# Performance work log

Hardware: AMD Instinct MI355X
Metric: run time of the kernel (lower is better)

## Reference

```python
import jax, jax.numpy as jnp
import numpy as np

N_HEADS = 16

def setup_inputs() -> dict:
    key = jax.random.key(0)
    ks = jax.random.split(key, 5)
    D = 1024
    B, T = 4, 1024
    scale = 1.0 / np.sqrt(D)
    x = jax.random.normal(ks[0], (B, T, D), dtype=jnp.float32)
    Wq = jax.random.normal(ks[1], (D, D), dtype=jnp.float32) * scale
    Wk = jax.random.normal(ks[2], (D, D), dtype=jnp.float32) * scale
    Wv = jax.random.normal(ks[3], (D, D), dtype=jnp.float32) * scale
    Wo = jax.random.normal(ks[4], (D, D), dtype=jnp.float32) * scale
    return {"x": x, "Wq": Wq, "Wk": Wk, "Wv": Wv, "Wo": Wo}


def reference(x, Wq, Wk, Wv, Wo):
    # FLA BasedLinearAttention (mode='chunk', normalize=True, scale=1) with
    # Taylor feature map phi(u) = [1, u/d^{1/4}, (u (x) u)/sqrt(2 d)], so
    # phi(q)·phi(k) = 1 + s + s^2/2 where s = (q·k)/sqrt(d).
    B, T, D = x.shape
    H = N_HEADS
    d = D // H  # head_dim == feature_dim
    # torch Linear: y = x @ W.T (bias=False in FLA proj layers)
    q = (x @ Wq.T).reshape(B, T, H, d).transpose(0, 2, 1, 3)  # b h t d
    k = (x @ Wk.T).reshape(B, T, H, d).transpose(0, 2, 1, 3)
    v = (x @ Wv.T).reshape(B, T, H, d).transpose(0, 2, 1, 3)
    s = jnp.einsum('bhtd,bhsd->bhts', q, k) / jnp.sqrt(jnp.float32(d))
    scores = 1.0 + s + 0.5 * s * s  # always > 0 (= ((s+1)^2+1)/2)
    causal = jnp.tril(jnp.ones((T, T), dtype=bool))
    scores = jnp.where(causal, scores, 0.0)
    num = jnp.einsum('bhts,bhsd->bhtd', scores, v)
    den = jnp.sum(scores, axis=-1, keepdims=True)
    o = num / den  # b h t d
    o = o.transpose(0, 2, 1, 3).reshape(B, T, D)  # b t (h d)
    return o @ Wo.T
```

## Files before the change

kernel.cpp:

```cpp
#include <hip/hip_runtime.h>

typedef unsigned short u16;
typedef __attribute__((ext_vector_type(8))) short bf16x8;
typedef __attribute__((ext_vector_type(8))) unsigned short u16x8;
typedef __attribute__((ext_vector_type(4))) float f32x4;

#define MFMA16(a, b, c) __builtin_amdgcn_mfma_f32_16x16x32_bf16((a), (b), (c), 0, 0, 0)

__device__ __forceinline__ void gll16(const void* g, void* l) {
    __builtin_amdgcn_global_load_lds(
        (const __attribute__((address_space(1))) unsigned int*)g,
        (__attribute__((address_space(3))) unsigned int*)l, 16, 0, 0);
}

__device__ __forceinline__ u16 f2b(float f) {
    unsigned int u = __float_as_uint(f);
    u += 0x7fffu + ((u >> 16) & 1u);
    return (u16)(u >> 16);
}

__device__ __forceinline__ unsigned int pkbf(float a, float b) {
    return (unsigned int)f2b(a) | ((unsigned int)f2b(b) << 16);
}

__global__ __launch_bounds__(256) void cast_x(const float* __restrict__ s,
                                              u16* __restrict__ d) {
    int i = (blockIdx.x * 256 + threadIdx.x) * 8;
    float4 a = *(const float4*)(s + i);
    float4 b = *(const float4*)(s + i + 4);
    uint4 r = make_uint4(pkbf(a.x, a.y), pkbf(a.z, a.w),
                         pkbf(b.x, b.y), pkbf(b.z, b.w));
    *(uint4*)(d + i) = r;
}

__global__ __launch_bounds__(256) void cast_w(const float* __restrict__ w0,
                                              const float* __restrict__ w1,
                                              const float* __restrict__ w2,
                                              const float* __restrict__ w3,
                                              u16* __restrict__ base) {
    const float* s = (blockIdx.y == 0) ? w0 : (blockIdx.y == 1) ? w1
                    : (blockIdx.y == 2) ? w2 : w3;
    u16* d = base + (size_t)blockIdx.y * 1048576;
    int i = (blockIdx.x * 256 + threadIdx.x) * 8;
    float4 a = *(const float4*)(s + i);
    float4 b = *(const float4*)(s + i + 4);
    uint4 r = make_uint4(pkbf(a.x, a.y), pkbf(a.z, a.w),
                         pkbf(b.x, b.y), pkbf(b.z, b.w));
    *(uint4*)(d + i) = r;
}

template <int BN, int OUT_BF16>
__global__ __launch_bounds__(256) void gemm_bt(const u16* __restrict__ A,
                                               const u16* __restrict__ W,
                                               void* __restrict__ Yv,
                                               int M, int N, int K) {
    __shared__ u16 As[128 * 32];
    __shared__ u16 Bs[BN * 32];
    constexpr int MI = (BN == 128) ? 4 : 2;
    const int t = threadIdx.x, w = t >> 6, lane = t & 63;
    const int quad = lane >> 4, m16 = lane & 15;
    const int wr = (BN == 128) ? ((w >> 1) * 64) : (w * 32);
    const int wc = (BN == 128) ? ((w & 1) * 64) : 0;
    const int row0 = blockIdx.x * 128, col0 = blockIdx.y * BN;
    const int srow = lane >> 2;
    const int scol = (lane & 3) * 8;

    f32x4 acc[MI][4];
#pragma unroll
    for (int i = 0; i < MI; ++i)
#pragma unroll
        for (int j = 0; j < 4; ++j) acc[i][j] = (f32x4){0.f, 0.f, 0.f, 0.f};

    for (int k0 = 0; k0 < K; k0 += 32) {
        if constexpr (BN == 128) {
#pragma unroll
            for (int cc = 0; cc < 2; ++cc) {
                const int c = w * 2 + cc;
                const int rr = c * 16 + srow;
                gll16(A + (size_t)(row0 + rr) * K + k0 + scol, &As[c * 512]);
                gll16(W + (size_t)(col0 + rr) * K + k0 + scol, &Bs[c * 512]);
            }
        } else {
#pragma unroll
            for (int cc = 0; cc < 2; ++cc) {
                const int c = w * 2 + cc;
                const int rr = c * 16 + srow;
                gll16(A + (size_t)(row0 + rr) * K + k0 + scol, &As[c * 512]);
            }
            {
                const int rr = w * 16 + srow;
                gll16(W + (size_t)(col0 + rr) * K + k0 + scol, &Bs[w * 512]);
            }
        }
        __syncthreads();
        bf16x8 af[MI], bf[4];
#pragma unroll
        for (int i = 0; i < MI; ++i)
            af[i] = *(const bf16x8*)&As[(wr + i * 16 + m16) * 32 + quad * 8];
#pragma unroll
        for (int j = 0; j < 4; ++j)
            bf[j] = *(const bf16x8*)&Bs[(wc + j * 16 + m16) * 32 + quad * 8];
#pragma unroll
        for (int i = 0; i < MI; ++i)
#pragma unroll
            for (int j = 0; j < 4; ++j) acc[i][j] = MFMA16(af[i], bf[j], acc[i][j]);
        __syncthreads();
    }
#pragma unroll
    for (int i = 0; i < MI; ++i)
#pragma unroll
        for (int j = 0; j < 4; ++j)
#pragma unroll
            for (int r = 0; r < 4; ++r) {
                const int rg = row0 + wr + i * 16 + quad * 4 + r;
                const int cg = col0 + wc + j * 16 + m16;
                if (OUT_BF16)
                    ((u16*)Yv)[(size_t)rg * N + cg] = f2b(acc[i][j][r]);
                else
                    ((float*)Yv)[(size_t)rg * N + cg] = acc[i][j][r];
            }
}

__global__ __launch_bounds__(256) void transpose_v(const u16* __restrict__ v,
                                                   u16* __restrict__ vT, int vstride) {
    __shared__ u16 tile[64][72];
    const int t = threadIdx.x;
    const int tt = blockIdx.x, h = blockIdx.y, b = blockIdx.z;
    {
        const int row = t >> 2, c4 = (t & 3) * 16;
        const u16* src = v + (size_t)(b * 1024 + tt * 64 + row) * vstride + h * 64 + c4;
        *(u16x8*)&tile[row][c4] = *(const u16x8*)src;
        *(u16x8*)&tile[row][c4 + 8] = *(const u16x8*)(src + 8);
    }
    __syncthreads();
    const int vd = t >> 2, tk = (t & 3) * 16;
    u16 tmp[16];
#pragma unroll
    for (int j = 0; j < 16; ++j) tmp[j] = tile[tk + j][vd];
    u16* dst = vT + (size_t)((b * 16 + h) * 64 + vd) * 1024 + tt * 64 + tk;
    *(u16x8*)dst = *(u16x8*)tmp;
    *(u16x8*)(dst + 8) = *(u16x8*)(tmp + 8);
}

__global__ __launch_bounds__(256) void based_attn(const u16* __restrict__ q,
                                                  const u16* __restrict__ k,
                                                  const u16* __restrict__ vT,
                                                  u16* __restrict__ o) {
    __shared__ u16 qs[2][128][32];
    __shared__ u16 ks[2][64][32];
    __shared__ u16 vs[2][64][32];
    __shared__ u16 Ss[2][128][32];

    const int t = threadIdx.x, w = t >> 6, lane = t & 63;
    const int quad = lane >> 4, m16 = lane & 15;
    const int qt2 = 7 - blockIdx.x;
    const int h = blockIdx.y, b = blockIdx.z;
    const int Q0 = qt2 * 128;
    const int srow = lane >> 2, s8 = (lane & 3) * 8;
    const int qw0 = Q0 + w * 32;

#pragma unroll
    for (int cc = 0; cc < 4; ++cc) {
        const int c = w * 4 + cc;
        const int dblk = c >> 3, rr = (c & 7) * 16 + srow;
        gll16(q + (size_t)(b * 1024 + Q0 + rr) * 3072 + h * 64 + dblk * 32 + s8,
              &qs[dblk][(c & 7) * 16][0]);
    }

    bf16x8 ones;
#pragma unroll
    for (int e = 0; e < 8; ++e) ones[e] = (short)0x3F80;

    f32x4 num[2][4], den[2];
#pragma unroll
    for (int i = 0; i < 2; ++i) {
        den[i] = (f32x4){0.f, 0.f, 0.f, 0.f};
#pragma unroll
        for (int j = 0; j < 4; ++j) num[i][j] = (f32x4){0.f, 0.f, 0.f, 0.f};
    }

    const int ktmax = 2 * qt2 + 1;
    for (int kt = 0; kt <= ktmax; ++kt) {
#pragma unroll
        for (int cc = 0; cc < 2; ++cc) {
            const int c = w * 2 + cc;
            const int blk = c >> 2, rr = (c & 3) * 16 + srow;
            gll16(k + (size_t)(b * 1024 + kt * 64 + rr) * 3072 + h * 64 + blk * 32 + s8,
                  &ks[blk][(c & 3) * 16][0]);
            gll16(vT + (size_t)((b * 16 + h) * 64 + rr) * 1024 + kt * 64 + blk * 32 + s8,
                  &vs[blk][(c & 3) * 16][0]);
        }
        __syncthreads();

        const bool active = (kt * 64 <= qw0 + 31);
        if (active) {
            f32x4 sacc[2][4];
#pragma unroll
            for (int iq = 0; iq < 2; ++iq)
#pragma unroll
                for (int jk = 0; jk < 4; ++jk) sacc[iq][jk] = (f32x4){0.f, 0.f, 0.f, 0.f};
#pragma unroll
            for (int kd = 0; kd < 2; ++kd) {
                bf16x8 af[4], qf[2];
#pragma unroll
                for (int jk = 0; jk < 4; ++jk)
                    af[jk] = *(const bf16x8*)&ks[kd][jk * 16 + m16][quad * 8];
#pragma unroll
                for (int iq = 0; iq < 2; ++iq)
                    qf[iq] = *(const bf16x8*)&qs[kd][w * 32 + iq * 16 + m16][quad * 8];
#pragma unroll
                for (int iq = 0; iq < 2; ++iq)
#pragma unroll
                    for (int jk = 0; jk < 4; ++jk)
                        sacc[iq][jk] = MFMA16(af[jk], qf[iq], sacc[iq][jk]);
            }
            const bool needMask = (kt * 64 + 63 > qw0);
#pragma unroll
            for (int iq = 0; iq < 2; ++iq) {
                const int qglob = qw0 + iq * 16 + m16;
#pragma unroll
                for (int jk = 0; jk < 4; ++jk) {
                    const int key0 = kt * 64 + jk * 16 + quad * 4;
                    float sc[4];
#pragma unroll
                    for (int r = 0; r < 4; ++r) {
                        const float u = fmaf(sacc[iq][jk][r], 0.125f, 1.0f);
                        sc[r] = fmaf(u * 0.5f, u, 0.5f);
                    }
                    if (needMask) {
#pragma unroll
                        for (int r = 0; r < 4; ++r)
                            if (key0 + r > qglob) sc[r] = 0.f;
                    }
                    const int kl = jk * 16 + quad * 4;
                    *(uint2*)&Ss[kl >> 5][w * 32 + iq * 16 + m16][kl & 31] =
                        make_uint2(pkbf(sc[0], sc[1]), pkbf(sc[2], sc[3]));
                }
            }
#pragma unroll
            for (int kb = 0; kb < 2; ++kb) {
                bf16x8 sf[2], vf[4];
#pragma unroll
                for (int i = 0; i < 2; ++i)
                    sf[i] = *(const bf16x8*)&Ss[kb][w * 32 + i * 16 + m16][quad * 8];
#pragma unroll
                for (int j = 0; j < 4; ++j)
                    vf[j] = *(const bf16x8*)&vs[kb][j * 16 + m16][quad * 8];
#pragma unroll
                for (int i = 0; i < 2; ++i) {
#pragma unroll
                    for (int j = 0; j < 4; ++j) num[i][j] = MFMA16(sf[i], vf[j], num[i][j]);
                    den[i] = MFMA16(sf[i], ones, den[i]);
                }
            }
        }
        __syncthreads();
    }

#pragma unroll
    for (int i = 0; i < 2; ++i)
#pragma unroll
        for (int r = 0; r < 4; ++r) {
            const float inv = 1.0f / den[i][r];
            const int tok = b * 1024 + Q0 + w * 32 + i * 16 + quad * 4 + r;
#pragma unroll
            for (int j = 0; j < 4; ++j)
                o[(size_t)tok * 1024 + h * 64 + j * 16 + m16] = f2b(num[i][j][r] * inv);
        }
}

extern "C" void kernel_launch(void* const* d_in, const int* in_sizes, int n_in,
                              void* d_out, int out_size, void* d_ws, size_t ws_size,
                              hipStream_t stream) {
    const float* x  = (const float*)d_in[0];
    const float* Wq = (const float*)d_in[1];
    const float* Wk = (const float*)d_in[2];
    const float* Wv = (const float*)d_in[3];
    const float* Wo = (const float*)d_in[4];
    float* out = (float*)d_out;

    const size_t MEL = 4096ull * 1024ull;
    u16* xb   = (u16*)d_ws;
    u16* Wqkv = xb + MEL;
    u16* Wob  = Wqkv + 3ull * 1024 * 1024;
    u16* qkv  = Wob + 1024ull * 1024;
    u16* vT   = qkv + 3ull * MEL;
    u16* o    = vT + MEL;

    cast_x<<<2048, 256, 0, stream>>>(x, xb);
    cast_w<<<dim3(512, 4), 256, 0, stream>>>(Wq, Wk, Wv, Wo, Wqkv);

    dim3 gq(32, 24);
    gemm_bt<128, 1><<<gq, 256, 0, stream>>>(xb, Wqkv, qkv, 4096, 3072, 1024);

    dim3 gt(16, 16, 4);
    transpose_v<<<gt, 256, 0, stream>>>(qkv + 2048, vT, 3072);

    dim3 ga(8, 16, 4);
    based_attn<<<ga, 256, 0, stream>>>(qkv, qkv + 1024, vT, o);

    dim3 go(32, 16);
    gemm_bt<64, 0><<<go, 256, 0, stream>>>(o, Wob, (void*)out, 4096, 1024, 1024);
}
```

Baseline: 187.3 us.

## Fuse casts, write V transposed from QKV GEMM, pair causal tiles in attention

Merges the x and weight cast kernels into one launch. The QKV GEMM epilogue now writes Q/K into a compact buffer and stores V directly in transposed layout, which removes the separate transpose kernel. The attention kernel now has each block own two 64-row query tiles (p and 15-p) so causal work is balanced across blocks, and it double-buffers K/V loads into LDS to overlap them with compute. The changes cut launches and global traffic, at the cost of strided uncoalesced 8-byte V stores and smaller per-wave query tiles.

```diff
diff --git a/kernel.cpp b/kernel.cpp
--- a/kernel.cpp
+++ b/kernel.cpp
@@ -23,37 +23,35 @@
     return (unsigned int)f2b(a) | ((unsigned int)f2b(b) << 16);
 }
 
-__global__ __launch_bounds__(256) void cast_x(const float* __restrict__ s,
-                                              u16* __restrict__ d) {
-    int i = (blockIdx.x * 256 + threadIdx.x) * 8;
+__global__ __launch_bounds__(256) void cast_all(const float* __restrict__ x,
+                                                const float* __restrict__ w0,
+                                                const float* __restrict__ w1,
+                                                const float* __restrict__ w2,
+                                                const float* __restrict__ w3,
+                                                u16* __restrict__ xb,
+                                                u16* __restrict__ wb) {
+    const int bid = blockIdx.x;
+    const float* s; u16* d; int off;
+    if (bid < 2048) { s = x; d = xb; off = bid; }
+    else {
+        const int wi = (bid - 2048) >> 9;
+        s = (wi == 0) ? w0 : (wi == 1) ? w1 : (wi == 2) ? w2 : w3;
+        d = wb + (size_t)wi * 1048576;
+        off = (bid - 2048) & 511;
+    }
+    const int i = (off * 256 + threadIdx.x) * 8;
     float4 a = *(const float4*)(s + i);
     float4 b = *(const float4*)(s + i + 4);
-    uint4 r = make_uint4(pkbf(a.x, a.y), pkbf(a.z, a.w),
-                         pkbf(b.x, b.y), pkbf(b.z, b.w));
-    *(uint4*)(d + i) = r;
-}
-
-__global__ __launch_bounds__(256) void cast_w(const float* __restrict__ w0,
-                                              const float* __restrict__ w1,
-                                              const float* __restrict__ w2,
-                                              const float* __restrict__ w3,
-                                              u16* __restrict__ base) {
-    const float* s = (blockIdx.y == 0) ? w0 : (blockIdx.y == 1) ? w1
-                    : (blockIdx.y == 2) ? w2 : w3;
-    u16* d = base + (size_t)blockIdx.y * 1048576;
-    int i = (blockIdx.x * 256 + threadIdx.x) * 8;
-    float4 a = *(const float4*)(s + i);
-    float4 b = *(const float4*)(s + i + 4);
-    uint4 r = make_uint4(pkbf(a.x, a.y), pkbf(a.z, a.w),
-                         pkbf(b.x, b.y), pkbf(b.z, b.w));
-    *(uint4*)(d + i) = r;
-}
-
-template <int BN, int OUT_BF16>
+    *(uint4*)(d + i) = make_uint4(pkbf(a.x, a.y), pkbf(a.z, a.w),
+                                  pkbf(b.x, b.y), pkbf(b.z, b.w));
+}
+
+template <int BN, int MODE>
 __global__ __launch_bounds__(256) void gemm_bt(const u16* __restrict__ A,
                                                const u16* __restrict__ W,
                                                void* __restrict__ Yv,
-                                               int M, int N, int K) {
+                                               u16* __restrict__ vT,
+                                               int K, int ldY) {
     __shared__ u16 As[128 * 32];
     __shared__ u16 Bs[BN * 32];
     constexpr int MI = (BN == 128) ? 4 : 2;
@@ -106,167 +104,166 @@
             for (int j = 0; j < 4; ++j) acc[i][j] = MFMA16(af[i], bf[j], acc[i][j]);
         __syncthreads();
     }
-#pragma unroll
-    for (int i = 0; i < MI; ++i)
-#pragma unroll
-        for (int j = 0; j < 4; ++j)
-#pragma unroll
-            for (int r = 0; r < 4; ++r) {
-                const int rg = row0 + wr + i * 16 + quad * 4 + r;
-                const int cg = col0 + wc + j * 16 + m16;
-                if (OUT_BF16)
-                    ((u16*)Yv)[(size_t)rg * N + cg] = f2b(acc[i][j][r]);
-                else
-                    ((float*)Yv)[(size_t)rg * N + cg] = acc[i][j][r];
-            }
-}
-
-__global__ __launch_bounds__(256) void transpose_v(const u16* __restrict__ v,
-                                                   u16* __restrict__ vT, int vstride) {
-    __shared__ u16 tile[64][72];
-    const int t = threadIdx.x;
-    const int tt = blockIdx.x, h = blockIdx.y, b = blockIdx.z;
-    {
-        const int row = t >> 2, c4 = (t & 3) * 16;
-        const u16* src = v + (size_t)(b * 1024 + tt * 64 + row) * vstride + h * 64 + c4;
-        *(u16x8*)&tile[row][c4] = *(const u16x8*)src;
-        *(u16x8*)&tile[row][c4 + 8] = *(const u16x8*)(src + 8);
-    }
-    __syncthreads();
-    const int vd = t >> 2, tk = (t & 3) * 16;
-    u16 tmp[16];
-#pragma unroll
-    for (int j = 0; j < 16; ++j) tmp[j] = tile[tk + j][vd];
-    u16* dst = vT + (size_t)((b * 16 + h) * 64 + vd) * 1024 + tt * 64 + tk;
-    *(u16x8*)dst = *(u16x8*)tmp;
-    *(u16x8*)(dst + 8) = *(u16x8*)(tmp + 8);
-}
-
-__global__ __launch_bounds__(256) void based_attn(const u16* __restrict__ q,
-                                                  const u16* __restrict__ k,
+    if constexpr (MODE == 0) {
+#pragma unroll
+        for (int i = 0; i < MI; ++i)
+#pragma unroll
+            for (int j = 0; j < 4; ++j)
+#pragma unroll
+                for (int r = 0; r < 4; ++r)
+                    ((float*)Yv)[(size_t)(row0 + wr + i * 16 + quad * 4 + r) * ldY +
+                                 col0 + wc + j * 16 + m16] = acc[i][j][r];
+    } else {
+        if (col0 < 2048) {
+            u16* qk = (u16*)Yv;
+#pragma unroll
+            for (int i = 0; i < MI; ++i)
+#pragma unroll
+                for (int j = 0; j < 4; ++j)
+#pragma unroll
+                    for (int r = 0; r < 4; ++r)
+                        qk[(size_t)(row0 + wr + i * 16 + quad * 4 + r) * 2048 +
+                           col0 + wc + j * 16 + m16] = f2b(acc[i][j][r]);
+        } else {
+#pragma unroll
+            for (int i = 0; i < MI; ++i) {
+                const int rbase = row0 + wr + i * 16;
+                const int bb = rbase >> 10;
+                const int tok0 = (rbase & 1023) + quad * 4;
+#pragma unroll
+                for (int j = 0; j < 4; ++j) {
+                    const int vTrow = bb * 1024 + (col0 + wc + j * 16 + m16 - 2048);
+                    *(uint2*)(vT + (size_t)vTrow * 1024 + tok0) =
+                        make_uint2(pkbf(acc[i][j][0], acc[i][j][1]),
+                                   pkbf(acc[i][j][2], acc[i][j][3]));
+                }
+            }
+        }
+    }
+}
+
+__global__ __launch_bounds__(256) void based_attn(const u16* __restrict__ qkm,
                                                   const u16* __restrict__ vT,
                                                   u16* __restrict__ o) {
-    __shared__ u16 qs[2][128][32];
-    __shared__ u16 ks[2][64][32];
-    __shared__ u16 vs[2][64][32];
-    __shared__ u16 Ss[2][128][32];
+    __shared__ u16 qsA[2][64][32];
+    __shared__ u16 qsB[2][64][32];
+    __shared__ u16 ks[2][2][64][32];
+    __shared__ u16 vs[2][2][64][32];
+    __shared__ u16 Ss[2][64][32];
 
     const int t = threadIdx.x, w = t >> 6, lane = t & 63;
     const int quad = lane >> 4, m16 = lane & 15;
-    const int qt2 = 7 - blockIdx.x;
-    const int h = blockIdx.y, b = blockIdx.z;
-    const int Q0 = qt2 * 128;
+    const int p = blockIdx.x, h = blockIdx.y, b = blockIdx.z;
+    const int tA = p, tB = 15 - p;
     const int srow = lane >> 2, s8 = (lane & 3) * 8;
-    const int qw0 = Q0 + w * 32;
+
+    const size_t qbase = (size_t)b * 1024 * 2048 + h * 64;
+    const size_t kbase = qbase + 1024;
+    const size_t vbase = ((size_t)b * 1024 + h * 64) * 1024;
 
 #pragma unroll
     for (int cc = 0; cc < 4; ++cc) {
         const int c = w * 4 + cc;
-        const int dblk = c >> 3, rr = (c & 7) * 16 + srow;
-        gll16(q + (size_t)(b * 1024 + Q0 + rr) * 3072 + h * 64 + dblk * 32 + s8,
-              &qs[dblk][(c & 7) * 16][0]);
+        const int tile = c >> 3, dblk = (c >> 2) & 1, rc = c & 3;
+        const int Q0 = (tile ? tB : tA) * 64;
+        gll16(qkm + qbase + (size_t)(Q0 + rc * 16 + srow) * 2048 + dblk * 32 + s8,
+              tile ? &qsB[dblk][rc * 16][0] : &qsA[dblk][rc * 16][0]);
+    }
+#pragma unroll
+    for (int cc = 0; cc < 2; ++cc) {
+        const int c = w * 2 + cc;
+        const int blk = c >> 2, rc = c & 3;
+        gll16(qkm + kbase + (size_t)(rc * 16 + srow) * 2048 + blk * 32 + s8,
+              &ks[0][blk][rc * 16][0]);
+        gll16(vT + vbase + (size_t)(rc * 16 + srow) * 1024 + blk * 32 + s8,
+              &vs[0][blk][rc * 16][0]);
     }
 
     bf16x8 ones;
 #pragma unroll
     for (int e = 0; e < 8; ++e) ones[e] = (short)0x3F80;
 
-    f32x4 num[2][4], den[2];
-#pragma unroll
-    for (int i = 0; i < 2; ++i) {
-        den[i] = (f32x4){0.f, 0.f, 0.f, 0.f};
-#pragma unroll
-        for (int j = 0; j < 4; ++j) num[i][j] = (f32x4){0.f, 0.f, 0.f, 0.f};
-    }
-
-    const int ktmax = 2 * qt2 + 1;
-    for (int kt = 0; kt <= ktmax; ++kt) {
-#pragma unroll
-        for (int cc = 0; cc < 2; ++cc) {
-            const int c = w * 2 + cc;
-            const int blk = c >> 2, rr = (c & 3) * 16 + srow;
-            gll16(k + (size_t)(b * 1024 + kt * 64 + rr) * 3072 + h * 64 + blk * 32 + s8,
-                  &ks[blk][(c & 3) * 16][0]);
-            gll16(vT + (size_t)((b * 16 + h) * 64 + rr) * 1024 + kt * 64 + blk * 32 + s8,
-                  &vs[blk][(c & 3) * 16][0]);
-        }
+    f32x4 numA[4], numB[4], denA, denB;
+    denA = denB = (f32x4){0.f, 0.f, 0.f, 0.f};
+#pragma unroll
+    for (int j = 0; j < 4; ++j) numA[j] = numB[j] = (f32x4){0.f, 0.f, 0.f, 0.f};
+
+#define TILE_COMPUTE(QS, NUM, DEN, DIAG)                                        \
+    {                                                                           \
+        f32x4 sacc[4];                                                          \
+        _Pragma("unroll")                                                       \
+        for (int jk = 0; jk < 4; ++jk) sacc[jk] = (f32x4){0.f, 0.f, 0.f, 0.f};  \
+        _Pragma("unroll")                                                       \
+        for (int kd = 0; kd < 2; ++kd) {                                        \
+            bf16x8 qf = *(const bf16x8*)&QS[kd][w * 16 + m16][quad * 8];        \
+            _Pragma("unroll")                                                   \
+            for (int jk = 0; jk < 4; ++jk) {                                    \
+                bf16x8 af = *(const bf16x8*)&ks[buf][kd][jk * 16 + m16][quad * 8]; \
+                sacc[jk] = MFMA16(af, qf, sacc[jk]);                            \
+            }                                                                   \
+        }                                                                       \
+        _Pragma("unroll")                                                       \
+        for (int jk = 0; jk < 4; ++jk) {                                        \
+            float sc[4];                                                        \
+            _Pragma("unroll")                                                   \
+            for (int r = 0; r < 4; ++r) {                                       \
+                const float u = fmaf(sacc[jk][r], 0.125f, 1.0f);                \
+                sc[r] = fmaf(u * 0.5f, u, 0.5f);                                \
+            }                                                                   \
+            if (DIAG) {                                                         \
+                const int key0 = jk * 16 + quad * 4, qr = w * 16 + m16;         \
+                _Pragma("unroll")                                               \
+                for (int r = 0; r < 4; ++r)                                     \
+                    if (key0 + r > qr) sc[r] = 0.f;                             \
+            }                                                                   \
+            const int kl = jk * 16 + quad * 4;                                  \
+            *(uint2*)&Ss[kl >> 5][w * 16 + m16][kl & 31] =                      \
+                make_uint2(pkbf(sc[0], sc[1]), pkbf(sc[2], sc[3]));             \
+        }                                                                       \
+        _Pragma("unroll")                                                       \
+        for (int kb = 0; kb < 2; ++kb) {                                        \
+            bf16x8 sf = *(const bf16x8*)&Ss[kb][w * 16 + m16][quad * 8];        \
+            _Pragma("unroll")                                                   \
+            for (int j = 0; j < 4; ++j) {                                       \
+                bf16x8 vf = *(const bf16x8*)&vs[buf][kb][j * 16 + m16][quad * 8]; \
+                NUM[j] = MFMA16(sf, vf, NUM[j]);                                \
+            }                                                                   \
+            DEN = MFMA16(sf, ones, DEN);                                        \
+        }                                                                       \
+    }
+
+    for (int kt = 0; kt <= tB; ++kt) {
+        const int buf = kt & 1;
         __syncthreads();
-
-        const bool active = (kt * 64 <= qw0 + 31);
-        if (active) {
-            f32x4 sacc[2][4];
-#pragma unroll
-            for (int iq = 0; iq < 2; ++iq)
-#pragma unroll
-                for (int jk = 0; jk < 4; ++jk) sacc[iq][jk] = (f32x4){0.f, 0.f, 0.f, 0.f};
-#pragma unroll
-            for (int kd = 0; kd < 2; ++kd) {
-                bf16x8 af[4], qf[2];
-#pragma unroll
-                for (int jk = 0; jk < 4; ++jk)
-                    af[jk] = *(const bf16x8*)&ks[kd][jk * 16 + m16][quad * 8];
-#pragma unroll
-                for (int iq = 0; iq < 2; ++iq)
-                    qf[iq] = *(const bf16x8*)&qs[kd][w * 32 + iq * 16 + m16][quad * 8];
-#pragma unroll
-                for (int iq = 0; iq < 2; ++iq)
-#pragma unroll
-                    for (int jk = 0; jk < 4; ++jk)
-                        sacc[iq][jk] = MFMA16(af[jk], qf[iq], sacc[iq][jk]);
-            }
-            const bool needMask = (kt * 64 + 63 > qw0);
-#pragma unroll
-            for (int iq = 0; iq < 2; ++iq) {
-                const int qglob = qw0 + iq * 16 + m16;
-#pragma unroll
-                for (int jk = 0; jk < 4; ++jk) {
-                    const int key0 = kt * 64 + jk * 16 + quad * 4;
-                    float sc[4];
-#pragma unroll
-                    for (int r = 0; r < 4; ++r) {
-                        const float u = fmaf(sacc[iq][jk][r], 0.125f, 1.0f);
-                        sc[r] = fmaf(u * 0.5f, u, 0.5f);
-                    }
-                    if (needMask) {
-#pragma unroll
-                        for (int r = 0; r < 4; ++r)
-                            if (key0 + r > qglob) sc[r] = 0.f;
-                    }
-                    const int kl = jk * 16 + quad * 4;
-                    *(uint2*)&Ss[kl >> 5][w * 32 + iq * 16 + m16][kl & 31] =
-                        make_uint2(pkbf(sc[0], sc[1]), pkbf(sc[2], sc[3]));
-                }
-            }
-#pragma unroll
-            for (int kb = 0; kb < 2; ++kb) {
-                bf16x8 sf[2], vf[4];
-#pragma unroll
-                for (int i = 0; i < 2; ++i)
-                    sf[i] = *(const bf16x8*)&Ss[kb][w * 32 + i * 16 + m16][quad * 8];
-#pragma unroll
-                for (int j = 0; j < 4; ++j)
-                    vf[j] = *(const bf16x8*)&vs[kb][j * 16 + m16][quad * 8];
-#pragma unroll
-                for (int i = 0; i < 2; ++i) {
-#pragma unroll
-                    for (int j = 0; j < 4; ++j) num[i][j] = MFMA16(sf[i], vf[j], num[i][j]);
-                    den[i] = MFMA16(sf[i], ones, den[i]);
-                }
-            }
-        }
-        __syncthreads();
-    }
-
-#pragma unroll
-    for (int i = 0; i < 2; ++i)
-#pragma unroll
-        for (int r = 0; r < 4; ++r) {
-            const float inv = 1.0f / den[i][r];
-            const int tok = b * 1024 + Q0 + w * 32 + i * 16 + quad * 4 + r;
-#pragma unroll
-            for (int j = 0; j < 4; ++j)
-                o[(size_t)tok * 1024 + h * 64 + j * 16 + m16] = f2b(num[i][j][r] * inv);
-        }
+        if (kt < tB) {
+            const int nb = buf ^ 1, kn = kt + 1;
+#pragma unroll
+            for (int cc = 0; cc < 2; ++cc) {
+                const int c = w * 2 + cc;
+                const int blk = c >> 2, rc = c & 3;
+                gll16(qkm + kbase + (size_t)(kn * 64 + rc * 16 + srow) * 2048 + blk * 32 + s8,
+                      &ks[nb][blk][rc * 16][0]);
+                gll16(vT + vbase + (size_t)(rc * 16 + srow) * 1024 + kn * 64 + blk * 32 + s8,
+                      &vs[nb][blk][rc * 16][0]);
+            }
+        }
+        TILE_COMPUTE(qsB, numB, denB, (kt == tB));
+        if (kt <= tA) TILE_COMPUTE(qsA, numA, denA, (kt == tA));
+    }
+#undef TILE_COMPUTE
+
+#pragma unroll
+    for (int r = 0; r < 4; ++r) {
+        const float invA = 1.0f / denA[r], invB = 1.0f / denB[r];
+        const int rowoff = w * 16 + quad * 4 + r;
+        const size_t tokA = (size_t)(b * 1024 + tA * 64 + rowoff);
+        const size_t tokB = (size_t)(b * 1024 + tB * 64 + rowoff);
+#pragma unroll
+        for (int j = 0; j < 4; ++j) {
+            o[tokA * 1024 + h * 64 + j * 16 + m16] = f2b(numA[j][r] * invA);
+            o[tokB * 1024 + h * 64 + j * 16 + m16] = f2b(numB[j][r] * invB);
+        }
+    }
 }
 
 extern "C" void kernel_launch(void* const* d_in, const int* in_sizes, int n_in,
@@ -283,22 +280,18 @@
     u16* xb   = (u16*)d_ws;
     u16* Wqkv = xb + MEL;
     u16* Wob  = Wqkv + 3ull * 1024 * 1024;
-    u16* qkv  = Wob + 1024ull * 1024;
-    u16* vT   = qkv + 3ull * MEL;
+    u16* qk   = Wob + 1024ull * 1024;
+    u16* vT   = qk + 2ull * MEL;
     u16* o    = vT + MEL;
 
-    cast_x<<<2048, 256, 0, stream>>>(x, xb);
-    cast_w<<<dim3(512, 4), 256, 0, stream>>>(Wq, Wk, Wv, Wo, Wqkv);
+    cast_all<<<4096, 256, 0, stream>>>(x, Wq, Wk, Wv, Wo, xb, Wqkv);
 
     dim3 gq(32, 24);
-    gemm_bt<128, 1><<<gq, 256, 0, stream>>>(xb, Wqkv, qkv, 4096, 3072, 1024);
-
-    dim3 gt(16, 16, 4);
-    transpose_v<<<gt, 256, 0, stream>>>(qkv + 2048, vT, 3072);
+    gemm_bt<128, 1><<<gq, 256, 0, stream>>>(xb, Wqkv, qk, vT, 1024, 2048);
 
     dim3 ga(8, 16, 4);
-    based_attn<<<ga, 256, 0, stream>>>(qkv, qkv + 1024, vT, o);
+    based_attn<<<ga, 256, 0, stream>>>(qk, vT, o);
 
     dim3 go(32, 16);
-    gemm_bt<64, 0><<<go, 256, 0, stream>>>(o, Wob, (void*)out, 4096, 1024, 1024);
-}
+    gemm_bt<64, 0><<<go, 256, 0, stream>>>(o, Wob, (void*)out, nullptr, 1024, 1024);
+}
```

Result: faster. 170.7 us (-8.9%).
